# Optimization experiments

Hardware: AMD Instinct MI355X
Metric: run time of the kernel (lower is better)

The kernel has to match this reference:

```python
import jax, jax.numpy as jnp
import numpy as np

N_NODES = 100000
N_EDGES = 1600000
BN_EPS = 1e-5


def _sage_conv(x, src, dst, Wl, Wr, b):
    # mean aggregation of neighbor (source) features onto destination nodes
    agg = jax.ops.segment_sum(x[src], dst, num_segments=x.shape[0])
    deg = jax.ops.segment_sum(jnp.ones((src.shape[0],), x.dtype), dst,
                              num_segments=x.shape[0])
    agg = agg / jnp.maximum(deg, 1.0)[:, None]
    # lin_l(agg) + lin_r(x); bias lives in lin_l (PyG SAGEConv default)
    return agg @ Wl + b + x @ Wr


def _batchnorm(x, gamma, beta):
    # training-mode BN over node dim, biased variance (torch BN forward)
    m = jnp.mean(x, axis=0)
    v = jnp.mean((x - m) ** 2, axis=0)
    return gamma * (x - m) * jax.lax.rsqrt(v + BN_EPS) + beta


def setup_inputs() -> dict:
    key = jax.random.key(0)
    ks = jax.random.split(key, 20)
    dims = [(128, 128), (128, 128), (128, 64)]  # (in, out) per layer
    inp = {
        "x": jax.random.normal(ks[0], (N_NODES, 128), dtype=jnp.float32),
        "edge_index": jax.random.randint(ks[1], (2, N_EDGES), 0, N_NODES,
                                         dtype=jnp.int64),
    }
    k = 2
    for i, (din, dout) in enumerate(dims):
        s = 1.0 / np.sqrt(din)
        inp[f"Wl{i}"] = jax.random.uniform(ks[k], (din, dout), jnp.float32, -s, s); k += 1
        inp[f"Wr{i}"] = jax.random.uniform(ks[k], (din, dout), jnp.float32, -s, s); k += 1
        inp[f"b{i}"] = jax.random.uniform(ks[k], (dout,), jnp.float32, -s, s); k += 1
        inp[f"gamma{i}"] = jnp.ones((dout,), jnp.float32)
        inp[f"beta{i}"] = jnp.zeros((dout,), jnp.float32)
    return inp


def reference(x, edge_index,
              Wl0, Wr0, b0, gamma0, beta0,
              Wl1, Wr1, b1, gamma1, beta1,
              Wl2, Wr2, b2, gamma2, beta2):
    src, dst = edge_index[0], edge_index[1]
    params = [(Wl0, Wr0, b0, gamma0, beta0),
              (Wl1, Wr1, b1, gamma1, beta1),
              (Wl2, Wr2, b2, gamma2, beta2)]
    h = x
    for i, (Wl, Wr, b, g, bt) in enumerate(params):
        h = _sage_conv(h, src, dst, Wl, Wr, b)
        h = _batchnorm(h, g, bt)
        if i < len(params) - 1:
            h = jax.nn.relu(h)
            # dropout is identity in this deterministic reference (eval mode)
    return h
```

## Files before the change

kernel.cpp:

```cpp
#include <hip/hip_runtime.h>
#include <hip/hip_bf16.h>

using bf16x8 = __attribute__((ext_vector_type(8))) short;
using f32x4  = __attribute__((ext_vector_type(4))) float;

__device__ __forceinline__ float b2f(unsigned short u) {
  union { unsigned int i; float f; } c;
  c.i = ((unsigned int)u) << 16;
  return c.f;
}
__device__ __forceinline__ unsigned short f2b(float f) {
  union { float f; unsigned int i; } c;
  c.f = f;
  unsigned int x = c.i;
  unsigned int r = x + 0x7fffu + ((x >> 16) & 1u);
  return (unsigned short)(r >> 16);
}

static constexpr int BCAP = 10240;
static constexpr int NBAGG = 1280;

__global__ __launch_bounds__(256) void k_part(const int* __restrict__ src,
                                              const int* __restrict__ dst,
                                              int* __restrict__ bcnt,
                                              unsigned int* __restrict__ barr,
                                              int e, int nbuk) {
  __shared__ int hist[256];
  __shared__ int base[256];
  __shared__ int h2[256];
  int t = threadIdx.x;
  hist[t] = 0;
  h2[t] = 0;
  __syncthreads();
  int e0 = blockIdx.x * 2048;
  int ms[8], md[8];
#pragma unroll
  for (int i = 0; i < 8; ++i) {
    int idx = e0 + i * 256 + t;
    if (idx < e) {
      ms[i] = src[idx];
      md[i] = dst[idx];
      atomicAdd(&hist[md[i] >> 9], 1);
    } else {
      md[i] = -1;
    }
  }
  __syncthreads();
  if (t < nbuk && hist[t] > 0) base[t] = atomicAdd(&bcnt[t], hist[t]);
  __syncthreads();
#pragma unroll
  for (int i = 0; i < 8; ++i) {
    if (md[i] >= 0) {
      int b = md[i] >> 9;
      int r = atomicAdd(&h2[b], 1);
      int pos = base[b] + r;
      if (pos < BCAP)
        barr[(size_t)b * BCAP + pos] =
            (unsigned int)ms[i] | ((unsigned int)(md[i] & 511) << 17);
    }
  }
}

__global__ __launch_bounds__(512) void k_bdeg(const int* __restrict__ bcnt,
                                              const unsigned int* __restrict__ barr,
                                              int* __restrict__ deg, int n) {
  __shared__ int cnt[512];
  int t = threadIdx.x;
  int b = blockIdx.x;
  cnt[t] = 0;
  __syncthreads();
  int c = bcnt[b];
  if (c > BCAP) c = BCAP;
  for (int i = t; i < c; i += 512)
    atomicAdd(&cnt[barr[(size_t)b * BCAP + i] >> 17], 1);
  __syncthreads();
  int node = b * 512 + t;
  if (node < n) deg[node] = cnt[t];
}

__global__ __launch_bounds__(256) void k_scan1(const int* __restrict__ deg,
                                               int* __restrict__ rs,
                                               int* __restrict__ bsum, int n) {
  __shared__ int s[256];
  int t = threadIdx.x;
  int i = blockIdx.x * 256 + t;
  int v = (i < n) ? deg[i] : 0;
  s[t] = v;
  __syncthreads();
  for (int off = 1; off < 256; off <<= 1) {
    int u = (t >= off) ? s[t - off] : 0;
    __syncthreads();
    s[t] += u;
    __syncthreads();
  }
  if (i < n) rs[i] = s[t] - v;
  if (t == 255) bsum[blockIdx.x] = s[255];
}

__global__ __launch_bounds__(512) void k_scan2(const int* __restrict__ bsum,
                                               int* __restrict__ boff, int nb) {
  __shared__ int s[512];
  int t = threadIdx.x;
  int v = (t < nb) ? bsum[t] : 0;
  s[t] = v;
  __syncthreads();
  for (int off = 1; off < 512; off <<= 1) {
    int u = (t >= off) ? s[t - off] : 0;
    __syncthreads();
    s[t] += u;
    __syncthreads();
  }
  if (t < nb) boff[t] = s[t] - v;
}

__global__ __launch_bounds__(256) void k_scan3(int* __restrict__ rs,
                                               const int* __restrict__ boff,
                                               int n, int e) {
  int i = blockIdx.x * blockDim.x + threadIdx.x;
  if (i < n) rs[i] = rs[i] + boff[i >> 8];
  if (i == 0) rs[n] = e;
}

__global__ __launch_bounds__(512) void k_place(const int* __restrict__ bcnt,
                                               const unsigned int* __restrict__ barr,
                                               const int* __restrict__ rs,
                                               int* __restrict__ csr, int n) {
  __shared__ int cnt[512];
  __shared__ int basep[512];
  int t = threadIdx.x;
  int b = blockIdx.x;
  int node = b * 512 + t;
  basep[t] = (node < n) ? rs[node] : 0;
  cnt[t] = 0;
  __syncthreads();
  int c = bcnt[b];
  if (c > BCAP) c = BCAP;
  for (int i = t; i < c; i += 512) {
    unsigned int v = barr[(size_t)b * BCAP + i];
    int loc = v >> 17;
    int r = atomicAdd(&cnt[loc], 1);
    csr[basep[loc] + r] = (int)(v & 0x1FFFFu);
  }
}

template <int NW>
__global__ __launch_bounds__(256) void k_wt(const float* __restrict__ Wl,
                                            const float* __restrict__ Wr,
                                            unsigned short* __restrict__ WT) {
  constexpr int DOUT = NW / 2;
  int idx = blockIdx.x * 256 + threadIdx.x;
  if (idx >= NW * 128) return;
  int nn = idx >> 7, k = idx & 127;
  float v = (nn < DOUT) ? Wl[(size_t)k * DOUT + nn]
                        : Wr[(size_t)k * DOUT + (nn - DOUT)];
  WT[idx] = f2b(v);
}

__global__ __launch_bounds__(256) void k_x0(const float* __restrict__ x,
                                            unsigned short* __restrict__ Xb,
                                            int n, int npad) {
  int total4 = npad * 32;
  for (int idx = blockIdx.x * 256 + threadIdx.x; idx < total4;
       idx += gridDim.x * 256) {
    int row = idx >> 5;
    ushort4 u = {0, 0, 0, 0};
    if (row < n) {
      float4 v = reinterpret_cast<const float4*>(x)[idx];
      u.x = f2b(v.x); u.y = f2b(v.y); u.z = f2b(v.z); u.w = f2b(v.w);
    }
    reinterpret_cast<ushort4*>(Xb)[idx] = u;
  }
}

__global__ __launch_bounds__(256) void k_bnrelu(const float* __restrict__ H,
                                                const float* __restrict__ sums,
                                                const float* __restrict__ gamma,
                                                const float* __restrict__ beta,
                                                unsigned short* __restrict__ Xb,
                                                int n, int npad) {
  float invn = 1.0f / (float)n;
  int total4 = npad * 32;
  for (int idx = blockIdx.x * 256 + threadIdx.x; idx < total4;
       idx += gridDim.x * 256) {
    int row = idx >> 5;
    ushort4 u = {0, 0, 0, 0};
    if (row < n) {
      int f0 = (idx & 31) * 4;
      float4 h = reinterpret_cast<const float4*>(H)[idx];
      float hv[4] = {h.x, h.y, h.z, h.w};
      unsigned short uu[4];
#pragma unroll
      for (int c = 0; c < 4; ++c) {
        int f = f0 + c;
        float m = sums[f] * invn;
        float var = sums[128 + f] * invn - m * m;
        float sc = gamma[f] * rsqrtf(var + 1e-5f);
        float sh = beta[f] - m * sc;
        uu[c] = f2b(fmaxf(hv[c] * sc + sh, 0.f));
      }
      u.x = uu[0]; u.y = uu[1]; u.z = uu[2]; u.w = uu[3];
    }
    reinterpret_cast<ushort4*>(Xb)[idx] = u;
  }
}

template <int NW>
__global__ __launch_bounds__(256) void k_gemm(
    const unsigned short* __restrict__ Xb, const unsigned short* __restrict__ WT,
    const float* __restrict__ bias, unsigned short* __restrict__ T16,
    float* __restrict__ H, int n) {
  constexpr int DOUT = NW / 2;
  constexpr int NT = NW / 16;
  constexpr int WS_BYTES = NW * 256;
  constexpr int EPR = NW + 4;
  constexpr int EPI_BYTES = 64 * EPR * 4;
  constexpr int SMEM_BYTES = (WS_BYTES > EPI_BYTES ? WS_BYTES : EPI_BYTES);
  __shared__ __align__(16) char smem[SMEM_BYTES];

  int t = threadIdx.x;
  int w = t >> 6;
  int l = t & 63;
  int lg = l >> 4;
  int ll = l & 15;
  int blk = blockIdx.x;
  int row16 = blk * 64 + w * 16;

  bf16x8 af[4];
  {
    const unsigned short* xrow = Xb + (size_t)(row16 + ll) * 128 + lg * 8;
#pragma unroll
    for (int s = 0; s < 4; ++s) {
      uint4 u = *reinterpret_cast<const uint4*>(xrow + s * 32);
      af[s] = __builtin_bit_cast(bf16x8, u);
    }
  }

  {
    const uint4* wg = reinterpret_cast<const uint4*>(WT);
    constexpr int C16 = NW * 16;
    for (int c = t; c < C16; c += 256) {
      int row = c >> 4;
      unsigned byte = ((unsigned)c << 4) ^ (((unsigned)row & 7u) << 4);
      *reinterpret_cast<uint4*>(smem + byte) = wg[c];
    }
  }
  __syncthreads();

  f32x4 acc[NT];
#pragma unroll
  for (int i = 0; i < NT; ++i) acc[i] = (f32x4){0.f, 0.f, 0.f, 0.f};

#pragma unroll
  for (int s = 0; s < 4; ++s) {
#pragma unroll
    for (int ct = 0; ct < NT; ++ct) {
      int row = ct * 16 + ll;
      unsigned byte =
          (unsigned)row * 256u + (((unsigned)(s * 64 + lg * 16)) ^
                                  (((unsigned)row & 7u) << 4));
      uint4 u = *reinterpret_cast<const uint4*>(smem + byte);
      bf16x8 bf = __builtin_bit_cast(bf16x8, u);
      acc[ct] = __builtin_amdgcn_mfma_f32_16x16x32_bf16(af[s], bf, acc[ct], 0, 0, 0);
    }
  }

  __syncthreads();
  float* epi = reinterpret_cast<float*>(smem);
#pragma unroll
  for (int ct = 0; ct < NT; ++ct) {
    int col = ct * 16 + ll;
#pragma unroll
    for (int r = 0; r < 4; ++r) {
      epi[(w * 16 + lg * 4 + r) * EPR + col] = acc[ct][r];
    }
  }
  __syncthreads();

  constexpr int CPR = NW / 4;
  constexpr int TCH = DOUT / 4;
#pragma unroll
  for (int i = 0; i < NW / 16; ++i) {
    int c = i * 256 + t;
    int row = c / CPR;
    int ch = c % CPR;
    int gr = blk * 64 + row;
    if (gr >= n) continue;
    float4 v = *reinterpret_cast<const float4*>(epi + row * EPR + ch * 4);
    if (ch < TCH) {
      ushort4 u;
      u.x = f2b(v.x); u.y = f2b(v.y); u.z = f2b(v.z); u.w = f2b(v.w);
      *reinterpret_cast<ushort4*>(T16 + (size_t)gr * DOUT + ch * 4) = u;
    } else {
      int cc = (ch - TCH) * 4;
      float4 bb = *reinterpret_cast<const float4*>(bias + cc);
      v.x += bb.x; v.y += bb.y; v.z += bb.z; v.w += bb.w;
      *reinterpret_cast<float4*>(H + (size_t)gr * DOUT + cc) = v;
    }
  }
}

__global__ __launch_bounds__(256) void k_agg128(const int* __restrict__ rs,
                                                const int* __restrict__ csr,
                                                const unsigned short* __restrict__ T,
                                                float* __restrict__ H,
                                                float* __restrict__ partials, int n) {
  int t = threadIdx.x;
  int grp = t >> 5, lane = t & 31;
  int off = lane * 4;
  float4 s4 = make_float4(0.f, 0.f, 0.f, 0.f);
  float4 q4 = make_float4(0.f, 0.f, 0.f, 0.f);
  for (int g = blockIdx.x * 8 + grp; g < n; g += NBAGG * 8) {
    int e0 = rs[g], e1 = rs[g + 1];
    int d = e1 - e0;
    float inv = 1.0f / (float)(d > 1 ? d : 1);
    float4 a = make_float4(0.f, 0.f, 0.f, 0.f);
    int e = e0;
    for (; e + 4 <= e1; e += 4) {
      int s0 = csr[e], s1 = csr[e + 1], s2 = csr[e + 2], s3 = csr[e + 3];
      ushort4 v0 = *reinterpret_cast<const ushort4*>(T + (size_t)s0 * 128 + off);
      ushort4 v1 = *reinterpret_cast<const ushort4*>(T + (size_t)s1 * 128 + off);
      ushort4 v2 = *reinterpret_cast<const ushort4*>(T + (size_t)s2 * 128 + off);
      ushort4 v3 = *reinterpret_cast<const ushort4*>(T + (size_t)s3 * 128 + off);
      a.x += (b2f(v0.x) + b2f(v1.x)) + (b2f(v2.x) + b2f(v3.x));
      a.y += (b2f(v0.y) + b2f(v1.y)) + (b2f(v2.y) + b2f(v3.y));
      a.z += (b2f(v0.z) + b2f(v1.z)) + (b2f(v2.z) + b2f(v3.z));
      a.w += (b2f(v0.w) + b2f(v1.w)) + (b2f(v2.w) + b2f(v3.w));
    }
    for (; e < e1; ++e) {
      int s = csr[e];
      ushort4 v = *reinterpret_cast<const ushort4*>(T + (size_t)s * 128 + off);
      a.x += b2f(v.x); a.y += b2f(v.y); a.z += b2f(v.z); a.w += b2f(v.w);
    }
    float4* hp = reinterpret_cast<float4*>(H + (size_t)g * 128 + off);
    float4 h = *hp;
    h.x += a.x * inv; h.y += a.y * inv; h.z += a.z * inv; h.w += a.w * inv;
    *hp = h;
    s4.x += h.x; s4.y += h.y; s4.z += h.z; s4.w += h.w;
    q4.x += h.x * h.x; q4.y += h.y * h.y; q4.z += h.z * h.z; q4.w += h.w * h.w;
  }
  __shared__ float ls[128];
  __shared__ float lq[128];
  if (t < 128) { ls[t] = 0.f; lq[t] = 0.f; }
  __syncthreads();
  atomicAdd(&ls[off + 0], s4.x); atomicAdd(&ls[off + 1], s4.y);
  atomicAdd(&ls[off + 2], s4.z); atomicAdd(&ls[off + 3], s4.w);
  atomicAdd(&lq[off + 0], q4.x); atomicAdd(&lq[off + 1], q4.y);
  atomicAdd(&lq[off + 2], q4.z); atomicAdd(&lq[off + 3], q4.w);
  __syncthreads();
  partials[(size_t)blockIdx.x * 256 + t] = (t < 128) ? ls[t] : lq[t - 128];
}

__global__ __launch_bounds__(256) void k_agg64(const int* __restrict__ rs,
                                               const int* __restrict__ csr,
                                               const unsigned short* __restrict__ T,
                                               float* __restrict__ H,
                                               float* __restrict__ partials, int n) {
  int t = threadIdx.x;
  int grp = t >> 4, lane = t & 15;
  int off = lane * 4;
  float4 s4 = make_float4(0.f, 0.f, 0.f, 0.f);
  float4 q4 = make_float4(0.f, 0.f, 0.f, 0.f);
  for (int g = blockIdx.x * 16 + grp; g < n; g += NBAGG * 16) {
    int e0 = rs[g], e1 = rs[g + 1];
    int d = e1 - e0;
    float inv = 1.0f / (float)(d > 1 ? d : 1);
    float4 a = make_float4(0.f, 0.f, 0.f, 0.f);
    int e = e0;
    for (; e + 4 <= e1; e += 4) {
      int s0 = csr[e], s1 = csr[e + 1], s2 = csr[e + 2], s3 = csr[e + 3];
      ushort4 v0 = *reinterpret_cast<const ushort4*>(T + (size_t)s0 * 64 + off);
      ushort4 v1 = *reinterpret_cast<const ushort4*>(T + (size_t)s1 * 64 + off);
      ushort4 v2 = *reinterpret_cast<const ushort4*>(T + (size_t)s2 * 64 + off);
      ushort4 v3 = *reinterpret_cast<const ushort4*>(T + (size_t)s3 * 64 + off);
      a.x += (b2f(v0.x) + b2f(v1.x)) + (b2f(v2.x) + b2f(v3.x));
      a.y += (b2f(v0.y) + b2f(v1.y)) + (b2f(v2.y) + b2f(v3.y));
      a.z += (b2f(v0.z) + b2f(v1.z)) + (b2f(v2.z) + b2f(v3.z));
      a.w += (b2f(v0.w) + b2f(v1.w)) + (b2f(v2.w) + b2f(v3.w));
    }
    for (; e < e1; ++e) {
      int s = csr[e];
      ushort4 v = *reinterpret_cast<const ushort4*>(T + (size_t)s * 64 + off);
      a.x += b2f(v.x); a.y += b2f(v.y); a.z += b2f(v.z); a.w += b2f(v.w);
    }
    float4* hp = reinterpret_cast<float4*>(H + (size_t)g * 64 + off);
    float4 h = *hp;
    h.x += a.x * inv; h.y += a.y * inv; h.z += a.z * inv; h.w += a.w * inv;
    *hp = h;
    s4.x += h.x; s4.y += h.y; s4.z += h.z; s4.w += h.w;
    q4.x += h.x * h.x; q4.y += h.y * h.y; q4.z += h.z * h.z; q4.w += h.w * h.w;
  }
  __shared__ float ls[64];
  __shared__ float lq[64];
  if (t < 64) { ls[t] = 0.f; lq[t] = 0.f; }
  __syncthreads();
  atomicAdd(&ls[off + 0], s4.x); atomicAdd(&ls[off + 1], s4.y);
  atomicAdd(&ls[off + 2], s4.z); atomicAdd(&ls[off + 3], s4.w);
  atomicAdd(&lq[off + 0], q4.x); atomicAdd(&lq[off + 1], q4.y);
  atomicAdd(&lq[off + 2], q4.z); atomicAdd(&lq[off + 3], q4.w);
  __syncthreads();
  if (t < 128)
    partials[(size_t)blockIdx.x * 128 + t] = (t < 64) ? ls[t] : lq[t - 64];
}

template <int DOUT>
__global__ __launch_bounds__(256) void k_red(const float* __restrict__ partials,
                                             float* __restrict__ bns) {
  int t = threadIdx.x;
  if (t >= 2 * DOUT) return;
  float acc = 0.f;
  for (int b = 0; b < NBAGG; ++b) acc += partials[(size_t)b * (2 * DOUT) + t];
  bns[t] = acc;
}

template <int DOUT, bool RELU>
__global__ __launch_bounds__(256) void k_bn_norm(const float* __restrict__ H,
                                                 const float* __restrict__ sums,
                                                 const float* __restrict__ gamma,
                                                 const float* __restrict__ beta,
                                                 float* __restrict__ O, int n) {
  float invn = 1.0f / (float)n;
  int total4 = n * (DOUT / 4);
  for (int idx = blockIdx.x * blockDim.x + threadIdx.x; idx < total4;
       idx += gridDim.x * blockDim.x) {
    int f0 = (idx % (DOUT / 4)) * 4;
    float4 h = reinterpret_cast<const float4*>(H)[idx];
    float hv[4] = {h.x, h.y, h.z, h.w};
    float o[4];
#pragma unroll
    for (int c = 0; c < 4; ++c) {
      int f = f0 + c;
      float m = sums[f] * invn;
      float var = sums[DOUT + f] * invn - m * m;
      float sc = gamma[f] * rsqrtf(var + 1e-5f);
      float sh = beta[f] - m * sc;
      float v = hv[c] * sc + sh;
      if (RELU) v = fmaxf(v, 0.f);
      o[c] = v;
    }
    reinterpret_cast<float4*>(O)[idx] = make_float4(o[0], o[1], o[2], o[3]);
  }
}

extern "C" void kernel_launch(void* const* d_in, const int* in_sizes, int n_in,
                              void* d_out, int out_size, void* d_ws, size_t ws_size,
                              hipStream_t stream) {
  const float* x = (const float*)d_in[0];
  const int* ei = (const int*)d_in[1];
  int n = in_sizes[0] / 128;
  int e = in_sizes[1] / 2;
  int npad = (n + 63) & ~63;
  int nbuk = (n + 511) >> 9;
  const int* src = ei;
  const int* dst = ei + e;

  char* p = (char*)d_ws;
  auto carve = [&](size_t bytes) {
    char* r = p;
    p += (bytes + 255) & ~(size_t)255;
    return r;
  };
  int* deg = (int*)carve((size_t)n * 4);
  int* rs = (int*)carve((size_t)(n + 1) * 4);
  int* bcnt = (int*)carve(1024);
  int* bsum = (int*)carve(4096);
  int* boff = (int*)carve(4096);
  float* bns = (float*)carve(1024);
  unsigned short* WTb = (unsigned short*)carve((size_t)256 * 128 * 2);
  float* partials = (float*)carve((size_t)NBAGG * 256 * 4);
  unsigned int* barr = (unsigned int*)carve((size_t)nbuk * BCAP * 4);
  int* csr = (int*)carve((size_t)e * 4);
  unsigned short* T16 = (unsigned short*)carve((size_t)n * 128 * 2);
  unsigned short* Xb = (unsigned short*)carve((size_t)npad * 128 * 2);
  float* Ha = (float*)carve((size_t)n * 128 * 4);
  float* Hb = (float*)carve((size_t)n * 128 * 4);

  hipMemsetAsync(bcnt, 0, (size_t)nbuk * 4, stream);
  int gA = (e + 2047) / 2048;
  int nb1 = (n + 255) / 256;
  k_part<<<gA, 256, 0, stream>>>(src, dst, bcnt, barr, e, nbuk);
  k_bdeg<<<nbuk, 512, 0, stream>>>(bcnt, barr, deg, n);
  k_scan1<<<nb1, 256, 0, stream>>>(deg, rs, bsum, n);
  k_scan2<<<1, 512, 0, stream>>>(bsum, boff, nb1);
  k_scan3<<<nb1, 256, 0, stream>>>(rs, boff, n, e);
  k_place<<<nbuk, 512, 0, stream>>>(bcnt, barr, rs, csr, n);

  int gg = npad / 64;
  int gcv = 4096;

  k_x0<<<gcv, 256, 0, stream>>>(x, Xb, n, npad);

  const float* prev_gm = nullptr;
  const float* prev_bt = nullptr;

  for (int layer = 0; layer < 3; ++layer) {
    const float* Wl = (const float*)d_in[2 + layer * 5];
    const float* Wr = (const float*)d_in[3 + layer * 5];
    const float* bb = (const float*)d_in[4 + layer * 5];
    const float* gm = (const float*)d_in[5 + layer * 5];
    const float* bt = (const float*)d_in[6 + layer * 5];

    if (layer == 0) {
      k_wt<256><<<128, 256, 0, stream>>>(Wl, Wr, WTb);
      k_gemm<256><<<gg, 256, 0, stream>>>(Xb, WTb, bb, T16, Ha, n);
      k_agg128<<<NBAGG, 256, 0, stream>>>(rs, csr, T16, Ha, partials, n);
      k_red<128><<<1, 256, 0, stream>>>(partials, bns);
    } else if (layer == 1) {
      k_bnrelu<<<gcv, 256, 0, stream>>>(Ha, bns, prev_gm, prev_bt, Xb, n, npad);
      k_wt<256><<<128, 256, 0, stream>>>(Wl, Wr, WTb);
      k_gemm<256><<<gg, 256, 0, stream>>>(Xb, WTb, bb, T16, Hb, n);
      k_agg128<<<NBAGG, 256, 0, stream>>>(rs, csr, T16, Hb, partials, n);
      k_red<128><<<1, 256, 0, stream>>>(partials, bns);
    } else {
      k_bnrelu<<<gcv, 256, 0, stream>>>(Hb, bns, prev_gm, prev_bt, Xb, n, npad);
      k_wt<128><<<64, 256, 0, stream>>>(Wl, Wr, WTb);
      k_gemm<128><<<gg, 256, 0, stream>>>(Xb, WTb, bb, T16, Ha, n);
      k_agg64<<<NBAGG, 256, 0, stream>>>(rs, csr, T16, Ha, partials, n);
      k_red<64><<<1, 256, 0, stream>>>(partials, bns);
      int total4 = n * 64 / 4;
      int gn = (total4 + 255) / 256;
      if (gn > 2048) gn = 2048;
      k_bn_norm<64, false><<<gn, 256, 0, stream>>>(Ha, bns, gm, bt, (float*)d_out, n);
    }
    prev_gm = gm;
    prev_bt = bt;
  }
}
```

Baseline: 533.3 us.

## Fuse BN+ReLU and bf16 conversion into GEMM prologue, parallelize stats reduction

The separate x-to-bf16 and BN+ReLU conversion kernels are removed. The GEMM now reads fp32 activations directly, applies BN scale/shift and ReLU, and packs to bf16 in registers, which saves a full write and re-read of the bf16 activation buffer per layer. The single-block stats reduction becomes a multi-block shuffle reduction, and the three weight transposes are merged into one launch. The 128-wide aggregation now uses 16-byte gathers with 16 lanes per node and more blocks; the trade-off is that the GEMM loads twice the bytes per activation row.

```diff
diff --git a/kernel.cpp b/kernel.cpp
--- a/kernel.cpp
+++ b/kernel.cpp
@@ -16,9 +16,21 @@
   unsigned int r = x + 0x7fffu + ((x >> 16) & 1u);
   return (unsigned short)(r >> 16);
 }
+__device__ __forceinline__ void decb8(uint4 u, float* f) {
+  union { uint4 v; unsigned short q[8]; } c;
+  c.v = u;
+#pragma unroll
+  for (int j = 0; j < 8; ++j) f[j] = b2f(c.q[j]);
+}
+__device__ __forceinline__ void decb4(uint2 u, float* f) {
+  union { uint2 v; unsigned short q[4]; } c;
+  c.v = u;
+#pragma unroll
+  for (int j = 0; j < 4; ++j) f[j] = b2f(c.q[j]);
+}
 
 static constexpr int BCAP = 10240;
-static constexpr int NBAGG = 1280;
+static constexpr int NBAGG = 2048;
 
 __global__ __launch_bounds__(256) void k_part(const int* __restrict__ src,
                                               const int* __restrict__ dst,
@@ -143,72 +155,32 @@
   }
 }
 
-template <int NW>
-__global__ __launch_bounds__(256) void k_wt(const float* __restrict__ Wl,
-                                            const float* __restrict__ Wr,
-                                            unsigned short* __restrict__ WT) {
-  constexpr int DOUT = NW / 2;
+__global__ __launch_bounds__(256) void k_wt_all(
+    const float* __restrict__ Wl0, const float* __restrict__ Wr0,
+    const float* __restrict__ Wl1, const float* __restrict__ Wr1,
+    const float* __restrict__ Wl2, const float* __restrict__ Wr2,
+    unsigned short* __restrict__ WT) {
   int idx = blockIdx.x * 256 + threadIdx.x;
-  if (idx >= NW * 128) return;
-  int nn = idx >> 7, k = idx & 127;
+  if (idx >= 81920) return;
+  int layer = idx >> 15;
+  int r = idx & 32767;
+  const float *Wl, *Wr;
+  int DOUT;
+  if (layer == 0) { Wl = Wl0; Wr = Wr0; DOUT = 128; }
+  else if (layer == 1) { Wl = Wl1; Wr = Wr1; DOUT = 128; }
+  else { Wl = Wl2; Wr = Wr2; DOUT = 64; }
+  int nn = r >> 7, k = r & 127;
   float v = (nn < DOUT) ? Wl[(size_t)k * DOUT + nn]
                         : Wr[(size_t)k * DOUT + (nn - DOUT)];
   WT[idx] = f2b(v);
 }
 
-__global__ __launch_bounds__(256) void k_x0(const float* __restrict__ x,
-                                            unsigned short* __restrict__ Xb,
-                                            int n, int npad) {
-  int total4 = npad * 32;
-  for (int idx = blockIdx.x * 256 + threadIdx.x; idx < total4;
-       idx += gridDim.x * 256) {
-    int row = idx >> 5;
-    ushort4 u = {0, 0, 0, 0};
-    if (row < n) {
-      float4 v = reinterpret_cast<const float4*>(x)[idx];
-      u.x = f2b(v.x); u.y = f2b(v.y); u.z = f2b(v.z); u.w = f2b(v.w);
-    }
-    reinterpret_cast<ushort4*>(Xb)[idx] = u;
-  }
-}
-
-__global__ __launch_bounds__(256) void k_bnrelu(const float* __restrict__ H,
-                                                const float* __restrict__ sums,
-                                                const float* __restrict__ gamma,
-                                                const float* __restrict__ beta,
-                                                unsigned short* __restrict__ Xb,
-                                                int n, int npad) {
-  float invn = 1.0f / (float)n;
-  int total4 = npad * 32;
-  for (int idx = blockIdx.x * 256 + threadIdx.x; idx < total4;
-       idx += gridDim.x * 256) {
-    int row = idx >> 5;
-    ushort4 u = {0, 0, 0, 0};
-    if (row < n) {
-      int f0 = (idx & 31) * 4;
-      float4 h = reinterpret_cast<const float4*>(H)[idx];
-      float hv[4] = {h.x, h.y, h.z, h.w};
-      unsigned short uu[4];
-#pragma unroll
-      for (int c = 0; c < 4; ++c) {
-        int f = f0 + c;
-        float m = sums[f] * invn;
-        float var = sums[128 + f] * invn - m * m;
-        float sc = gamma[f] * rsqrtf(var + 1e-5f);
-        float sh = beta[f] - m * sc;
-        uu[c] = f2b(fmaxf(hv[c] * sc + sh, 0.f));
-      }
-      u.x = uu[0]; u.y = uu[1]; u.z = uu[2]; u.w = uu[3];
-    }
-    reinterpret_cast<ushort4*>(Xb)[idx] = u;
-  }
-}
-
-template <int NW>
+template <int NW, bool FUSE>
 __global__ __launch_bounds__(256) void k_gemm(
-    const unsigned short* __restrict__ Xb, const unsigned short* __restrict__ WT,
-    const float* __restrict__ bias, unsigned short* __restrict__ T16,
-    float* __restrict__ H, int n) {
+    const float* __restrict__ Xf, const unsigned short* __restrict__ WT,
+    const float* __restrict__ bias, const float* __restrict__ bns,
+    const float* __restrict__ gamma, const float* __restrict__ beta,
+    unsigned short* __restrict__ T16, float* __restrict__ H, int n) {
   constexpr int DOUT = NW / 2;
   constexpr int NT = NW / 16;
   constexpr int WS_BYTES = NW * 256;
@@ -216,6 +188,7 @@
   constexpr int EPI_BYTES = 64 * EPR * 4;
   constexpr int SMEM_BYTES = (WS_BYTES > EPI_BYTES ? WS_BYTES : EPI_BYTES);
   __shared__ __align__(16) char smem[SMEM_BYTES];
+  __shared__ float scsh[256];
 
   int t = threadIdx.x;
   int w = t >> 6;
@@ -225,22 +198,53 @@
   int blk = blockIdx.x;
   int row16 = blk * 64 + w * 16;
 
+  if constexpr (FUSE) {
+    if (t < 128) {
+      float invn = 1.0f / (float)n;
+      float m = bns[t] * invn;
+      float var = bns[128 + t] * invn - m * m;
+      float sc = gamma[t] * rsqrtf(var + 1e-5f);
+      scsh[t] = sc;
+      scsh[128 + t] = beta[t] - m * sc;
+    }
+    __syncthreads();
+  }
+
+  int row = row16 + ll;
+  bool valid = row < n;
+  const float* xrow = Xf + (size_t)row * 128 + lg * 8;
   bf16x8 af[4];
-  {
-    const unsigned short* xrow = Xb + (size_t)(row16 + ll) * 128 + lg * 8;
-#pragma unroll
-    for (int s = 0; s < 4; ++s) {
-      uint4 u = *reinterpret_cast<const uint4*>(xrow + s * 32);
-      af[s] = __builtin_bit_cast(bf16x8, u);
-    }
+#pragma unroll
+  for (int s = 0; s < 4; ++s) {
+    float v[8];
+    if (valid) {
+      float4 a = *reinterpret_cast<const float4*>(xrow + s * 32);
+      float4 b = *reinterpret_cast<const float4*>(xrow + s * 32 + 4);
+      v[0] = a.x; v[1] = a.y; v[2] = a.z; v[3] = a.w;
+      v[4] = b.x; v[5] = b.y; v[6] = b.z; v[7] = b.w;
+    } else {
+#pragma unroll
+      for (int j = 0; j < 8; ++j) v[j] = 0.f;
+    }
+    if constexpr (FUSE) {
+#pragma unroll
+      for (int j = 0; j < 8; ++j) {
+        int f = lg * 8 + s * 32 + j;
+        v[j] = fmaxf(v[j] * scsh[f] + scsh[128 + f], 0.f);
+      }
+    }
+    union { unsigned short q[8]; bf16x8 bv; } pk;
+#pragma unroll
+    for (int j = 0; j < 8; ++j) pk.q[j] = f2b(v[j]);
+    af[s] = pk.bv;
   }
 
   {
     const uint4* wg = reinterpret_cast<const uint4*>(WT);
     constexpr int C16 = NW * 16;
     for (int c = t; c < C16; c += 256) {
-      int row = c >> 4;
-      unsigned byte = ((unsigned)c << 4) ^ (((unsigned)row & 7u) << 4);
+      int rw = c >> 4;
+      unsigned byte = ((unsigned)c << 4) ^ (((unsigned)rw & 7u) << 4);
       *reinterpret_cast<uint4*>(smem + byte) = wg[c];
     }
   }
@@ -254,10 +258,10 @@
   for (int s = 0; s < 4; ++s) {
 #pragma unroll
     for (int ct = 0; ct < NT; ++ct) {
-      int row = ct * 16 + ll;
+      int rw = ct * 16 + ll;
       unsigned byte =
-          (unsigned)row * 256u + (((unsigned)(s * 64 + lg * 16)) ^
-                                  (((unsigned)row & 7u) << 4));
+          (unsigned)rw * 256u + (((unsigned)(s * 64 + lg * 16)) ^
+                                 (((unsigned)rw & 7u) << 4));
       uint4 u = *reinterpret_cast<const uint4*>(smem + byte);
       bf16x8 bf = __builtin_bit_cast(bf16x8, u);
       acc[ct] = __builtin_amdgcn_mfma_f32_16x16x32_bf16(af[s], bf, acc[ct], 0, 0, 0);
@@ -281,11 +285,11 @@
 #pragma unroll
   for (int i = 0; i < NW / 16; ++i) {
     int c = i * 256 + t;
-    int row = c / CPR;
+    int rw = c / CPR;
     int ch = c % CPR;
-    int gr = blk * 64 + row;
+    int gr = blk * 64 + rw;
     if (gr >= n) continue;
-    float4 v = *reinterpret_cast<const float4*>(epi + row * EPR + ch * 4);
+    float4 v = *reinterpret_cast<const float4*>(epi + rw * EPR + ch * 4);
     if (ch < TCH) {
       ushort4 u;
       u.x = f2b(v.x); u.y = f2b(v.y); u.z = f2b(v.z); u.w = f2b(v.w);
@@ -305,47 +309,60 @@
                                                 float* __restrict__ H,
                                                 float* __restrict__ partials, int n) {
   int t = threadIdx.x;
-  int grp = t >> 5, lane = t & 31;
-  int off = lane * 4;
-  float4 s4 = make_float4(0.f, 0.f, 0.f, 0.f);
-  float4 q4 = make_float4(0.f, 0.f, 0.f, 0.f);
-  for (int g = blockIdx.x * 8 + grp; g < n; g += NBAGG * 8) {
+  int grp = t >> 4, lane = t & 15;
+  int off = lane * 8;
+  float s8[8], q8[8];
+#pragma unroll
+  for (int j = 0; j < 8; ++j) { s8[j] = 0.f; q8[j] = 0.f; }
+  for (int g = blockIdx.x * 16 + grp; g < n; g += NBAGG * 16) {
     int e0 = rs[g], e1 = rs[g + 1];
     int d = e1 - e0;
     float inv = 1.0f / (float)(d > 1 ? d : 1);
-    float4 a = make_float4(0.f, 0.f, 0.f, 0.f);
+    float a[8];
+#pragma unroll
+    for (int j = 0; j < 8; ++j) a[j] = 0.f;
     int e = e0;
     for (; e + 4 <= e1; e += 4) {
       int s0 = csr[e], s1 = csr[e + 1], s2 = csr[e + 2], s3 = csr[e + 3];
-      ushort4 v0 = *reinterpret_cast<const ushort4*>(T + (size_t)s0 * 128 + off);
-      ushort4 v1 = *reinterpret_cast<const ushort4*>(T + (size_t)s1 * 128 + off);
-      ushort4 v2 = *reinterpret_cast<const ushort4*>(T + (size_t)s2 * 128 + off);
-      ushort4 v3 = *reinterpret_cast<const ushort4*>(T + (size_t)s3 * 128 + off);
-      a.x += (b2f(v0.x) + b2f(v1.x)) + (b2f(v2.x) + b2f(v3.x));
-      a.y += (b2f(v0.y) + b2f(v1.y)) + (b2f(v2.y) + b2f(v3.y));
-      a.z += (b2f(v0.z) + b2f(v1.z)) + (b2f(v2.z) + b2f(v3.z));
-      a.w += (b2f(v0.w) + b2f(v1.w)) + (b2f(v2.w) + b2f(v3.w));
+      uint4 u0 = *reinterpret_cast<const uint4*>(T + (size_t)s0 * 128 + off);
+      uint4 u1 = *reinterpret_cast<const uint4*>(T + (size_t)s1 * 128 + off);
+      uint4 u2 = *reinterpret_cast<const uint4*>(T + (size_t)s2 * 128 + off);
+      uint4 u3 = *reinterpret_cast<const uint4*>(T + (size_t)s3 * 128 + off);
+      float f0[8], f1[8], f2[8], f3[8];
+      decb8(u0, f0); decb8(u1, f1); decb8(u2, f2); decb8(u3, f3);
+#pragma unroll
+      for (int j = 0; j < 8; ++j) a[j] += (f0[j] + f1[j]) + (f2[j] + f3[j]);
     }
     for (; e < e1; ++e) {
       int s = csr[e];
-      ushort4 v = *reinterpret_cast<const ushort4*>(T + (size_t)s * 128 + off);
-      a.x += b2f(v.x); a.y += b2f(v.y); a.z += b2f(v.z); a.w += b2f(v.w);
-    }
-    float4* hp = reinterpret_cast<float4*>(H + (size_t)g * 128 + off);
-    float4 h = *hp;
-    h.x += a.x * inv; h.y += a.y * inv; h.z += a.z * inv; h.w += a.w * inv;
-    *hp = h;
-    s4.x += h.x; s4.y += h.y; s4.z += h.z; s4.w += h.w;
-    q4.x += h.x * h.x; q4.y += h.y * h.y; q4.z += h.z * h.z; q4.w += h.w * h.w;
+      uint4 u = *reinterpret_cast<const uint4*>(T + (size_t)s * 128 + off);
+      float f[8];
+      decb8(u, f);
+#pragma unroll
+      for (int j = 0; j < 8; ++j) a[j] += f[j];
+    }
+    float4* hp0 = reinterpret_cast<float4*>(H + (size_t)g * 128 + off);
+    float4* hp1 = hp0 + 1;
+    float4 h0 = *hp0, h1 = *hp1;
+    float h[8] = {h0.x, h0.y, h0.z, h0.w, h1.x, h1.y, h1.z, h1.w};
+#pragma unroll
+    for (int j = 0; j < 8; ++j) {
+      h[j] += a[j] * inv;
+      s8[j] += h[j];
+      q8[j] += h[j] * h[j];
+    }
+    *hp0 = make_float4(h[0], h[1], h[2], h[3]);
+    *hp1 = make_float4(h[4], h[5], h[6], h[7]);
   }
   __shared__ float ls[128];
   __shared__ float lq[128];
   if (t < 128) { ls[t] = 0.f; lq[t] = 0.f; }
   __syncthreads();
-  atomicAdd(&ls[off + 0], s4.x); atomicAdd(&ls[off + 1], s4.y);
-  atomicAdd(&ls[off + 2], s4.z); atomicAdd(&ls[off + 3], s4.w);
-  atomicAdd(&lq[off + 0], q4.x); atomicAdd(&lq[off + 1], q4.y);
-  atomicAdd(&lq[off + 2], q4.z); atomicAdd(&lq[off + 3], q4.w);
+#pragma unroll
+  for (int j = 0; j < 8; ++j) {
+    atomicAdd(&ls[off + j], s8[j]);
+    atomicAdd(&lq[off + j], q8[j]);
+  }
   __syncthreads();
   partials[(size_t)blockIdx.x * 256 + t] = (t < 128) ? ls[t] : lq[t - 128];
 }
@@ -358,58 +375,70 @@
   int t = threadIdx.x;
   int grp = t >> 4, lane = t & 15;
   int off = lane * 4;
-  float4 s4 = make_float4(0.f, 0.f, 0.f, 0.f);
-  float4 q4 = make_float4(0.f, 0.f, 0.f, 0.f);
+  float s4[4], q4[4];
+#pragma unroll
+  for (int j = 0; j < 4; ++j) { s4[j] = 0.f; q4[j] = 0.f; }
   for (int g = blockIdx.x * 16 + grp; g < n; g += NBAGG * 16) {
     int e0 = rs[g], e1 = rs[g + 1];
     int d = e1 - e0;
     float inv = 1.0f / (float)(d > 1 ? d : 1);
-    float4 a = make_float4(0.f, 0.f, 0.f, 0.f);
+    float a[4];
+#pragma unroll
+    for (int j = 0; j < 4; ++j) a[j] = 0.f;
     int e = e0;
     for (; e + 4 <= e1; e += 4) {
       int s0 = csr[e], s1 = csr[e + 1], s2 = csr[e + 2], s3 = csr[e + 3];
-      ushort4 v0 = *reinterpret_cast<const ushort4*>(T + (size_t)s0 * 64 + off);
-      ushort4 v1 = *reinterpret_cast<const ushort4*>(T + (size_t)s1 * 64 + off);
-      ushort4 v2 = *reinterpret_cast<const ushort4*>(T + (size_t)s2 * 64 + off);
-      ushort4 v3 = *reinterpret_cast<const ushort4*>(T + (size_t)s3 * 64 + off);
-      a.x += (b2f(v0.x) + b2f(v1.x)) + (b2f(v2.x) + b2f(v3.x));
-      a.y += (b2f(v0.y) + b2f(v1.y)) + (b2f(v2.y) + b2f(v3.y));
-      a.z += (b2f(v0.z) + b2f(v1.z)) + (b2f(v2.z) + b2f(v3.z));
-      a.w += (b2f(v0.w) + b2f(v1.w)) + (b2f(v2.w) + b2f(v3.w));
+      uint2 u0 = *reinterpret_cast<const uint2*>(T + (size_t)s0 * 64 + off);
+      uint2 u1 = *reinterpret_cast<const uint2*>(T + (size_t)s1 * 64 + off);
+      uint2 u2 = *reinterpret_cast<const uint2*>(T + (size_t)s2 * 64 + off);
+      uint2 u3 = *reinterpret_cast<const uint2*>(T + (size_t)s3 * 64 + off);
+      float f0[4], f1[4], f2[4], f3[4];
+      decb4(u0, f0); decb4(u1, f1); decb4(u2, f2); decb4(u3, f3);
+#pragma unroll
+      for (int j = 0; j < 4; ++j) a[j] += (f0[j] + f1[j]) + (f2[j] + f3[j]);
     }
     for (; e < e1; ++e) {
       int s = csr[e];
-      ushort4 v = *reinterpret_cast<const ushort4*>(T + (size_t)s * 64 + off);
-      a.x += b2f(v.x); a.y += b2f(v.y); a.z += b2f(v.z); a.w += b2f(v.w);
+      uint2 u = *reinterpret_cast<const uint2*>(T + (size_t)s * 64 + off);
+      float f[4];
+      decb4(u, f);
+#pragma unroll
+      for (int j = 0; j < 4; ++j) a[j] += f[j];
     }
     float4* hp = reinterpret_cast<float4*>(H + (size_t)g * 64 + off);
-    float4 h = *hp;
-    h.x += a.x * inv; h.y += a.y * inv; h.z += a.z * inv; h.w += a.w * inv;
-    *hp = h;
-    s4.x += h.x; s4.y += h.y; s4.z += h.z; s4.w += h.w;
-    q4.x += h.x * h.x; q4.y += h.y * h.y; q4.z += h.z * h.z; q4.w += h.w * h.w;
+    float4 hv = *hp;
+    float h[4] = {hv.x, hv.y, hv.z, hv.w};
+#pragma unroll
+    for (int j = 0; j < 4; ++j) {
+      h[j] += a[j] * inv;
+      s4[j] += h[j];
+      q4[j] += h[j] * h[j];
+    }
+    *hp = make_float4(h[0], h[1], h[2], h[3]);
   }
   __shared__ float ls[64];
   __shared__ float lq[64];
   if (t < 64) { ls[t] = 0.f; lq[t] = 0.f; }
   __syncthreads();
-  atomicAdd(&ls[off + 0], s4.x); atomicAdd(&ls[off + 1], s4.y);
-  atomicAdd(&ls[off + 2], s4.z); atomicAdd(&ls[off + 3], s4.w);
-  atomicAdd(&lq[off + 0], q4.x); atomicAdd(&lq[off + 1], q4.y);
-  atomicAdd(&lq[off + 2], q4.z); atomicAdd(&lq[off + 3], q4.w);
+#pragma unroll
+  for (int j = 0; j < 4; ++j) {
+    atomicAdd(&ls[off + j], s4[j]);
+    atomicAdd(&lq[off + j], q4[j]);
+  }
   __syncthreads();
   if (t < 128)
-    partials[(size_t)blockIdx.x * 128 + t] = (t < 64) ? ls[t] : lq[t - 64];
-}
-
-template <int DOUT>
-__global__ __launch_bounds__(256) void k_red(const float* __restrict__ partials,
-                                             float* __restrict__ bns) {
-  int t = threadIdx.x;
-  if (t >= 2 * DOUT) return;
+    partials[(size_t)blockIdx.x * 256 + t] = (t < 64) ? ls[t] : lq[t - 64];
+}
+
+__global__ __launch_bounds__(64) void k_red(const float* __restrict__ partials,
+                                            float* __restrict__ bns) {
+  int f = blockIdx.x;
+  int j = threadIdx.x;
   float acc = 0.f;
-  for (int b = 0; b < NBAGG; ++b) acc += partials[(size_t)b * (2 * DOUT) + t];
-  bns[t] = acc;
+  for (int b = j; b < NBAGG; b += 64) acc += partials[(size_t)b * 256 + f];
+#pragma unroll
+  for (int off = 32; off > 0; off >>= 1) acc += __shfl_down(acc, off);
+  if (j == 0) bns[f] = acc;
 }
 
 template <int DOUT, bool RELU>
@@ -465,16 +494,31 @@
   int* bsum = (int*)carve(4096);
   int* boff = (int*)carve(4096);
   float* bns = (float*)carve(1024);
-  unsigned short* WTb = (unsigned short*)carve((size_t)256 * 128 * 2);
+  unsigned short* WTall = (unsigned short*)carve((size_t)81920 * 2);
   float* partials = (float*)carve((size_t)NBAGG * 256 * 4);
   unsigned int* barr = (unsigned int*)carve((size_t)nbuk * BCAP * 4);
   int* csr = (int*)carve((size_t)e * 4);
   unsigned short* T16 = (unsigned short*)carve((size_t)n * 128 * 2);
-  unsigned short* Xb = (unsigned short*)carve((size_t)npad * 128 * 2);
   float* Ha = (float*)carve((size_t)n * 128 * 4);
   float* Hb = (float*)carve((size_t)n * 128 * 4);
 
-  hipMemsetAsync(bcnt, 0, (size_t)nbuk * 4, stream);
+  const float* Wl0 = (const float*)d_in[2];
+  const float* Wr0 = (const float*)d_in[3];
+  const float* b0 = (const float*)d_in[4];
+  const float* gm0 = (const float*)d_in[5];
+  const float* bt0 = (const float*)d_in[6];
+  const float* Wl1 = (const float*)d_in[7];
+  const float* Wr1 = (const float*)d_in[8];
+  const float* b1 = (const float*)d_in[9];
+  const float* gm1 = (const float*)d_in[10];
+  const float* bt1 = (const float*)d_in[11];
+  const float* Wl2 = (const float*)d_in[12];
+  const float* Wr2 = (const float*)d_in[13];
+  const float* b2 = (const float*)d_in[14];
+  const float* gm2 = (const float*)d_in[15];
+  const float* bt2 = (const float*)d_in[16];
+
+  hipMemsetAsync(bcnt, 0, 1024, stream);
   int gA = (e + 2047) / 2048;
   int nb1 = (n + 255) / 256;
   k_part<<<gA, 256, 0, stream>>>(src, dst, bcnt, barr, e, nbuk);
@@ -484,44 +528,21 @@
   k_scan3<<<nb1, 256, 0, stream>>>(rs, boff, n, e);
   k_place<<<nbuk, 512, 0, stream>>>(bcnt, barr, rs, csr, n);
 
+  k_wt_all<<<320, 256, 0, stream>>>(Wl0, Wr0, Wl1, Wr1, Wl2, Wr2, WTall);
+
   int gg = npad / 64;
-  int gcv = 4096;
-
-  k_x0<<<gcv, 256, 0, stream>>>(x, Xb, n, npad);
-
-  const float* prev_gm = nullptr;
-  const float* prev_bt = nullptr;
-
-  for (int layer = 0; layer < 3; ++layer) {
-    const float* Wl = (const float*)d_in[2 + layer * 5];
-    const float* Wr = (const float*)d_in[3 + layer * 5];
-    const float* bb = (const float*)d_in[4 + layer * 5];
-    const float* gm = (const float*)d_in[5 + layer * 5];
-    const float* bt = (const float*)d_in[6 + layer * 5];
-
-    if (layer == 0) {
-      k_wt<256><<<128, 256, 0, stream>>>(Wl, Wr, WTb);
-      k_gemm<256><<<gg, 256, 0, stream>>>(Xb, WTb, bb, T16, Ha, n);
-      k_agg128<<<NBAGG, 256, 0, stream>>>(rs, csr, T16, Ha, partials, n);
-      k_red<128><<<1, 256, 0, stream>>>(partials, bns);
-    } else if (layer == 1) {
-      k_bnrelu<<<gcv, 256, 0, stream>>>(Ha, bns, prev_gm, prev_bt, Xb, n, npad);
-      k_wt<256><<<128, 256, 0, stream>>>(Wl, Wr, WTb);
-      k_gemm<256><<<gg, 256, 0, stream>>>(Xb, WTb, bb, T16, Hb, n);
-      k_agg128<<<NBAGG, 256, 0, stream>>>(rs, csr, T16, Hb, partials, n);
-      k_red<128><<<1, 256, 0, stream>>>(partials, bns);
-    } else {
-      k_bnrelu<<<gcv, 256, 0, stream>>>(Hb, bns, prev_gm, prev_bt, Xb, n, npad);
-      k_wt<128><<<64, 256, 0, stream>>>(Wl, Wr, WTb);
-      k_gemm<128><<<gg, 256, 0, stream>>>(Xb, WTb, bb, T16, Ha, n);
-      k_agg64<<<NBAGG, 256, 0, stream>>>(rs, csr, T16, Ha, partials, n);
-      k_red<64><<<1, 256, 0, stream>>>(partials, bns);
-      int total4 = n * 64 / 4;
-      int gn = (total4 + 255) / 256;
-      if (gn > 2048) gn = 2048;
-      k_bn_norm<64, false><<<gn, 256, 0, stream>>>(Ha, bns, gm, bt, (float*)d_out, n);
-    }
-    prev_gm = gm;
-    prev_bt = bt;
-  }
-}
+
+  k_gemm<256, false><<<gg, 256, 0, stream>>>(x, WTall, b0, bns, gm0, bt0, T16, Ha, n);
+  k_agg128<<<NBAGG, 256, 0, stream>>>(rs, csr, T16, Ha, partials, n);
+  k_red<<<256, 64, 0, stream>>>(partials, bns);
+  k_gemm<256, true><<<gg, 256, 0, stream>>>(Ha, WTall + 32768, b1, bns, gm0, bt0, T16, Hb, n);
+  k_agg128<<<NBAGG, 256, 0, stream>>>(rs, csr, T16, Hb, partials, n);
+  k_red<<<256, 64, 0, stream>>>(partials, bns);
+  k_gemm<128, true><<<gg, 256, 0, stream>>>(Hb, WTall + 65536, b2, bns, gm1, bt1, T16, Ha, n);
+  k_agg64<<<NBAGG, 256, 0, stream>>>(rs, csr, T16, Ha, partials, n);
+  k_red<<<128, 64, 0, stream>>>(partials, bns);
+  int total4 = n * 64 / 4;
+  int gn = (total4 + 255) / 256;
+  if (gn > 2048) gn = 2048;
+  k_bn_norm<64, false><<<gn, 256, 0, stream>>>(Ha, bns, gm2, bt2, (float*)d_out, n);
+}
```

New measurement: 492.1 us. 7.7% less time.
